# Performance work log

Measured on AMD Instinct MI355X. Metric: run time of the kernel, lower is better.

Reference implementation:

```python
import jax, jax.numpy as jnp
import numpy as np

B, C, H, W = 2, 256, 56, 56
NH = 8
HD = C // NH
SCALE = HD ** -0.5
BN_EPS = 1e-5


def _linear(x, w, b=None):
    y = jnp.einsum('...i,oi->...o', x, w)
    return y + b if b is not None else y


def _dwconv3(v, w, b):
    # depthwise 3x3, stride 1, pad 1
    y = jax.lax.conv_general_dilated(v, w, (1, 1), 'SAME',
                                     dimension_numbers=('NCHW', 'OIHW', 'NCHW'),
                                     feature_group_count=C)
    return y + b[None, :, None, None]


def _spectral(x, context, qw, kvw, pw, pb, dww, dwb):
    # SpectralCrossAttention, sr_ratio=1 path
    xt = jnp.transpose(x, (0, 2, 3, 1))                    # B,H,W,C
    q = jnp.transpose(_linear(xt, qw), (0, 3, 1, 2))       # B,C,H,W
    ct = jnp.transpose(context, (0, 2, 3, 1))
    kv = _linear(ct, kvw)                                  # B,H,W,2C -> split [2,C]
    k = jnp.transpose(kv[..., :C], (0, 3, 1, 2))
    v = jnp.transpose(kv[..., C:], (0, 3, 1, 2))
    v_local = _dwconv3(v, dww, dwb)
    qf = jnp.fft.rfft2(q, s=(H, W), axes=(-2, -1), norm='ortho')
    kf = jnp.fft.rfft2(k, s=(H, W), axes=(-2, -1), norm='ortho')
    attn_map = jnp.fft.irfft2(qf * kf, s=(H, W), axes=(-2, -1), norm='ortho')
    out = attn_map * v + v_local
    out = _linear(jnp.transpose(out, (0, 2, 3, 1)), pw, pb)
    return jnp.transpose(out, (0, 3, 1, 2))


def _token(x, context, qw, kvw, pw, pb, cw):
    # TokenSpectralResidualCrossAttention, sr_ratio=1 path (de_conv = Identity)
    N = H * W
    xt = jnp.transpose(x.reshape(B, C, N), (0, 2, 1))       # B,N,C
    ct = jnp.transpose(context.reshape(B, C, N), (0, 2, 1))
    q = jnp.transpose(_linear(xt, qw).reshape(B, N, NH, HD), (0, 2, 1, 3))  # B,NH,N,HD
    kv = _linear(ct, kvw).reshape(B, N, 2, NH, HD)
    k = jnp.transpose(kv[:, :, 0], (0, 2, 1, 3))
    v = jnp.transpose(kv[:, :, 1], (0, 2, 1, 3))            # B,NH,N,HD
    attn = jax.nn.softmax(jnp.einsum('bhnd,bhmd->bhnm', q, k) * SCALE, axis=-1)
    x_attn = jnp.transpose(jnp.einsum('bhnm,bhmd->bhnd', attn, v), (0, 2, 1, 3)).reshape(B, N, C)
    v_img = jnp.transpose(v, (0, 1, 3, 2)).reshape(B, C, H, W)
    vf = jnp.fft.rfft2(v_img, s=(H, W), axes=(-2, -1), norm='ortho')
    weight = cw[..., 0] + 1j * cw[..., 1]                   # C,H,W//2+1 complex
    v_res = jnp.fft.irfft2(vf * weight[None], s=(H, W), axes=(-2, -1), norm='ortho')
    v_res = jnp.transpose(v_res.reshape(B, C, N), (0, 2, 1))
    out = _linear(x_attn + v_res, pw, pb)
    return jnp.transpose(out, (0, 2, 1)).reshape(B, C, H, W)


def _fuse(os_, ot, g_w1, g_bn_g, g_bn_b, g_w2, g_b2):
    # spatial_gate: Conv1x1(2C->C, no bias) -> BN(eval: mean0/var1) -> ReLU -> Conv1x1(C->1) -> Sigmoid
    g_in = jnp.concatenate([os_, ot], axis=1)               # B,2C,H,W
    h = jnp.einsum('oc,bchw->bohw', g_w1, g_in)
    h = h / jnp.sqrt(1.0 + BN_EPS) * g_bn_g[None, :, None, None] + g_bn_b[None, :, None, None]
    h = jax.nn.relu(h)
    gate = jax.nn.sigmoid(jnp.einsum('oc,bchw->bohw', g_w2, h) + g_b2[None, :, None, None])
    return gate * os_ + (1.0 - gate) * ot


def setup_inputs():
    key = jax.random.key(0)
    ks = jax.random.split(key, 14)
    p = lambda i, shape, s=0.02: jax.random.normal(ks[i], shape, jnp.float32) * s
    return {
        'x': jax.random.normal(ks[0], (B, C, H, W), jnp.float32),
        'context': jax.random.normal(ks[1], (B, C, H, W), jnp.float32),
        's_q_w': p(2, (C, C)),
        's_kv_w': p(3, (2 * C, C)),
        's_proj_w': p(4, (C, C)),
        's_proj_b': jnp.zeros((C,), jnp.float32),
        's_dw_w': p(5, (C, 1, 3, 3), float(np.sqrt(2.0 / 9.0))),
        's_dw_b': jnp.zeros((C,), jnp.float32),
        't_q_w': p(6, (C, C)),
        't_kv_w': p(7, (2 * C, C)),
        't_proj_w': p(8, (C, C)),
        't_proj_b': jnp.zeros((C,), jnp.float32),
        't_cw': p(9, (C, H, W // 2 + 1, 2)),
        'g_w1': p(10, (C, 2 * C), float(np.sqrt(2.0 / C))),
        'g_bn_g': jnp.ones((C,), jnp.float32),
        'g_bn_b': jnp.zeros((C,), jnp.float32),
        'g_w2': p(11, (1, C), float(np.sqrt(2.0 / C))),
        'g_b2': jnp.zeros((1,), jnp.float32),
    }


def reference(x, context, s_q_w, s_kv_w, s_proj_w, s_proj_b, s_dw_w, s_dw_b,
              t_q_w, t_kv_w, t_proj_w, t_proj_b, t_cw,
              g_w1, g_bn_g, g_bn_b, g_w2, g_b2):
    os_ = _spectral(x, context, s_q_w, s_kv_w, s_proj_w, s_proj_b, s_dw_w, s_dw_b)
    ot = _token(x, context, t_q_w, t_kv_w, t_proj_w, t_proj_b, t_cw)
    return _fuse(os_, ot, g_w1, g_bn_g, g_bn_b, g_w2, g_b2)
```

## Files before the change

### kernel.cpp

```cpp
#include <hip/hip_runtime.h>

namespace {
constexpr int kB = 2;
constexpr int kC = 256;
constexpr int kH = 56;
constexpr int kW = 56;
constexpr int kN = kH * kW;
constexpr int kNH = 8;
constexpr int kHD = 32;
constexpr int kNF = kW / 2 + 1;
constexpr int kSpec = kH * kNF;
constexpr long kCN = (long)kC * kN;
constexpr float kAttScale = 0.17677669529663687f;
constexpr float kLog2e = 1.4426950408889634f;
constexpr float kAng = 6.283185307179586f / 56.0f;
constexpr int TW1F = 0;
constexpr int TW2F = 8192;
constexpr int TW1I = 12288;
constexpr int TW2I = 20480;
constexpr int TWTOT = 24576;
}

typedef __attribute__((ext_vector_type(8))) short short8;
typedef __attribute__((ext_vector_type(4))) float float4v;

union Frag {
    short8 s;
    unsigned short u[8];
    uint2 u2[2];
    uint4 u4;
};

__device__ __forceinline__ unsigned short f2b(float f) {
    unsigned u = __float_as_uint(f);
    return (unsigned short)((u + 0x7FFFu + ((u >> 16) & 1u)) >> 16);
}
__device__ __forceinline__ float b2f(unsigned short u) {
    return __uint_as_float((unsigned)u << 16);
}
__device__ __forceinline__ unsigned f2b_pk(float a, float b) {
    unsigned ua = __float_as_uint(a); ua = (ua + 0x7FFFu + ((ua >> 16) & 1u)) >> 16;
    unsigned ub = __float_as_uint(b); ub = (ub + 0x7FFFu + ((ub >> 16) & 1u)) >> 16;
    return ua | (ub << 16);
}
__device__ __forceinline__ unsigned pk_trunc(float a, float b) {
    return (__float_as_uint(a) >> 16) | (__float_as_uint(b) & 0xFFFF0000u);
}
__device__ __forceinline__ uint4 pk8(const float* v) {
    return make_uint4(f2b_pk(v[0], v[1]), f2b_pk(v[2], v[3]),
                      f2b_pk(v[4], v[5]), f2b_pk(v[6], v[7]));
}

__global__ __launch_bounds__(256)
void twiddle_init_kernel(unsigned short* __restrict__ tw)
{
    int idx = blockIdx.x * 256 + threadIdx.x;
    if (idx >= TWTOT) return;
    float val = 0.f;
    if (idx < TW2F) {
        int r = idx >> 6, c = idx & 63;
        if (c < 56) {
            if (r < 56)       val = cosf(kAng * (float)((r * c) % 56));
            else if (r < 112) val = sinf(kAng * (float)(((r - 56) * c) % 56));
        }
    } else if (idx < TW1I) {
        int t = idx - TW2F; int r = t >> 6, c = t & 63;
        if (c < 56) {
            if (r < 29)                  val = cosf(kAng * (float)((r * c) % 56));
            else if (r >= 32 && r < 61)  val = sinf(kAng * (float)(((r - 32) * c) % 56));
        }
    } else if (idx < TW2I) {
        int t = idx - TW1I; int r = t >> 6, c = t & 63;
        if (c < 56) {
            if (r < 56)                  val = cosf(kAng * (float)((r * c) % 56));
            else if (r >= 64 && r < 120) val = sinf(kAng * (float)(((r - 64) * c) % 56));
        }
    } else {
        int t = idx - TW2I; int x = t >> 6, c = t & 63;
        if (x < 56 && c < 58) {
            int v = c >> 1;
            float wv = ((v == 0) || (v == 28)) ? 1.f : 2.f;
            float a = kAng * (float)((v * x) % 56);
            val = (c & 1) ? (-wv * sinf(a)) : (wv * cosf(a));
        }
    }
    tw[idx] = f2b(val);
}

__device__ void dft_fwd_body(char* smem, int bx,
                             const float* __restrict__ s0, const float* __restrict__ s1,
                             const float* __restrict__ s2, float* __restrict__ d0,
                             float* __restrict__ d1, float* __restrict__ d2,
                             const unsigned short* __restrict__ tw)
{
    const int which = bx >> 9, ch = bx & 511;
    const int b = ch >> 8, c = ch & 255;
    const float* src; long stride; float* spec;
    if (which == 0)      { src = s0; stride = kCN;     spec = d0; }
    else if (which == 1) { src = s1; stride = 2 * kCN; spec = d1; }
    else                 { src = s2; stride = 2 * kCN; spec = d2; }
    const float* img = src + (long)b * stride + (long)c * kN;

    unsigned short (*Gb)[72]    = (unsigned short(*)[72])smem;
    unsigned short (*imgT)[72]  = (unsigned short(*)[72])(smem + 18432);
    unsigned short (*Yb)[116]   = (unsigned short(*)[116])(smem + 18432);

    const int tid = threadIdx.x;
    const int wave = tid >> 6, lane = tid & 63;
    const int ln = lane & 15, qd = lane >> 4;

    for (int i = tid; i < 64 * 72; i += 256) {
        int r = i / 72, cc = i - r * 72;
        if (r >= 56 || cc >= 56) imgT[r][cc] = 0;
    }
    for (int i = tid; i < kN; i += 256) {
        int y = i / 56, x = i - y * 56;
        imgT[x][y] = f2b(img[i]);
    }
    __syncthreads();

    float4v acc1[2][4];
#pragma unroll
    for (int m = 0; m < 2; ++m)
#pragma unroll
        for (int n = 0; n < 4; ++n) acc1[m][n] = (float4v){0.f, 0.f, 0.f, 0.f};
#pragma unroll
    for (int ks = 0; ks < 2; ++ks) {
        Frag a[2], bf[4];
#pragma unroll
        for (int m = 0; m < 2; ++m)
            a[m].u4 = *(const uint4*)(tw + TW1F + ((2 * wave + m) * 16 + ln) * 64 + ks * 32 + qd * 8);
#pragma unroll
        for (int n = 0; n < 4; ++n)
            bf[n].u4 = *(const uint4*)&imgT[n * 16 + ln][ks * 32 + qd * 8];
#pragma unroll
        for (int m = 0; m < 2; ++m)
#pragma unroll
            for (int n = 0; n < 4; ++n)
                acc1[m][n] = __builtin_amdgcn_mfma_f32_16x16x32_bf16(a[m].s, bf[n].s, acc1[m][n], 0, 0, 0);
    }
#pragma unroll
    for (int m = 0; m < 2; ++m)
#pragma unroll
        for (int n = 0; n < 4; ++n)
#pragma unroll
            for (int r = 0; r < 4; ++r)
                Gb[(2 * wave + m) * 16 + qd * 4 + r][n * 16 + ln] = f2b(acc1[m][n][r]);
    __syncthreads();

    float4v acc2[7];
#pragma unroll
    for (int n = 0; n < 7; ++n) acc2[n] = (float4v){0.f, 0.f, 0.f, 0.f};
#pragma unroll
    for (int ks = 0; ks < 2; ++ks) {
        Frag a;
        a.u4 = *(const uint4*)(tw + TW2F + (wave * 16 + ln) * 64 + ks * 32 + qd * 8);
#pragma unroll
        for (int n = 0; n < 7; ++n) {
            Frag bb;
            bb.u4 = *(const uint4*)&Gb[n * 16 + ln][ks * 32 + qd * 8];
            acc2[n] = __builtin_amdgcn_mfma_f32_16x16x32_bf16(a.s, bb.s, acc2[n], 0, 0, 0);
        }
    }
#pragma unroll
    for (int n = 0; n < 7; ++n)
#pragma unroll
        for (int r = 0; r < 4; ++r)
            Yb[wave * 16 + qd * 4 + r][n * 16 + ln] = f2b(acc2[n][r]);
    __syncthreads();

    float2* outp = (float2*)spec + (long)ch * kSpec;
    for (int i = tid; i < kSpec; i += 256) {
        int u = i / kNF, v = i - u * kNF;
        float Qr = b2f(Yb[v][u]) - b2f(Yb[32 + v][56 + u]);
        float Qi = -b2f(Yb[32 + v][u]) - b2f(Yb[v][56 + u]);
        outp[i] = make_float2(Qr, Qi);
    }
}

__device__ void prepack_body(char* smem, int blk, const float* __restrict__ tkv,
                             unsigned short* __restrict__ Kp,
                             unsigned short* __restrict__ Vp)
{
    const int i = blk % 49;
    const int h = (blk / 49) & 7;
    const int b = blk / (49 * 8);
    const float* kb = tkv + (long)b * 2 * kCN + (long)h * kHD * kN;
    const float* vb = kb + kCN;
    const int tid = threadIdx.x;

    float (*Ks)[72] = (float(*)[72])smem;
#pragma unroll
    for (int j = 0; j < 8; ++j) {
        int e = tid + j * 256;
        int d = e >> 6, c = e & 63;
        Ks[d][c] = kb[(long)d * kN + i * 64 + c];
    }
    __syncthreads();
    {
        int tl = tid >> 6, lnn = (tid >> 2) & 15, qdd = tid & 3;
        float v[8];
#pragma unroll
        for (int j = 0; j < 8; ++j) v[j] = Ks[qdd * 8 + j][tl * 16 + lnn];
        unsigned short* dst = Kp + ((long)(b * 8 + h) * 196 + 4 * i + tl) * 512 + lnn * 32 + qdd * 8;
        *(uint4*)dst = pk8(v);
    }
    {
        int g = tid >> 7, dh = (tid >> 6) & 1, lnn = (tid >> 2) & 15, qdd = tid & 3;
        int d = dh * 16 + lnn;
        const float* src = vb + (long)d * kN + i * 64 + g * 32 + qdd * 8;
        float v[8];
        *(float4*)&v[0] = *(const float4*)src;
        *(float4*)&v[4] = *(const float4*)(src + 4);
        unsigned short* dst = Vp + ((long)(b * 8 + h) * 49 + i) * 2048 + ((g * 2 + dh) * 16 + lnn) * 32 + qdd * 8;
        *(uint4*)dst = pk8(v);
    }
}

__global__ __launch_bounds__(256)
void fwd3_prepack_kernel(const float* __restrict__ s0, const float* __restrict__ s1,
                         const float* __restrict__ s2, float* __restrict__ d0,
                         float* __restrict__ d1, float* __restrict__ d2,
                         const unsigned short* __restrict__ tw,
                         const float* __restrict__ tkv,
                         unsigned short* __restrict__ Kp, unsigned short* __restrict__ Vp)
{
    __shared__ __align__(16) char smem[33280];
    if (blockIdx.x < 1536)
        dft_fwd_body(smem, blockIdx.x, s0, s1, s2, d0, d1, d2, tw);
    else
        prepack_body(smem, blockIdx.x - 1536, tkv, Kp, Vp);
}

__global__ __launch_bounds__(256)
void dft_inv_mfma2(const float* __restrict__ fQ, const float* __restrict__ fK,
                   const float* __restrict__ fV, const float* __restrict__ cw,
                   float* __restrict__ dst1, float* __restrict__ dst2,
                   const float* __restrict__ skvp, const float* __restrict__ dww,
                   const float* __restrict__ dwb, const unsigned short* __restrict__ tw)
{
    const int unit = blockIdx.x >> 9;
    const int ch = blockIdx.x & 511;
    const int b = ch >> 8, c = ch & 255;
    __shared__ __align__(16) char smem[27648];
    unsigned short (*Pb)[72]  = (unsigned short(*)[72])smem;
    unsigned short (*Yb)[72]  = (unsigned short(*)[72])(smem + 9216);
    unsigned short (*T2)[72]  = (unsigned short(*)[72])smem;
    float (*svs)[65]          = (float(*)[65])(smem + 9216);

    const int tid = threadIdx.x;
    const int wave = tid >> 6, lane = tid & 63;
    const int ln = lane & 15, qd = lane >> 4;

    const float2* Pin; const float2* Min; float scale; float* dst;
    if (unit == 0) {
        Pin = (const float2*)fQ + (long)ch * kSpec;
        Min = (const float2*)fK + (long)ch * kSpec;
        scale = 1.0f / 175616.0f; dst = dst1;
    } else {
        Pin = (const float2*)fV + (long)ch * kSpec;
        Min = (const float2*)cw + (long)c * kSpec;
        scale = 1.0f / 3136.0f; dst = dst2;
    }

    for (int i = tid; i < 64 * 72; i += 256) {
        int r = i / 72, cc = i - r * 72;
        if (r >= 58 || cc >= 56) Pb[r][cc] = 0;
    }
    for (int i = tid; i < kSpec; i += 256) {
        int u = i / kNF, v = i - u * kNF;
        float2 p = Pin[i];
        float2 m = Min[i];
        float pr = (p.x * m.x - p.y * m.y) * scale;
        float pi = (p.x * m.y + p.y * m.x) * scale;
        Pb[2 * v][u]     = f2b(pr);
        Pb[2 * v + 1][u] = f2b(pi);
    }
    __syncthreads();

    float4v acc1[2][4];
#pragma unroll
    for (int m = 0; m < 2; ++m)
#pragma unroll
        for (int n = 0; n < 4; ++n) acc1[m][n] = (float4v){0.f, 0.f, 0.f, 0.f};
#pragma unroll
    for (int ks = 0; ks < 2; ++ks) {
        Frag a[2], bf[4];
#pragma unroll
        for (int m = 0; m < 2; ++m)
            a[m].u4 = *(const uint4*)(tw + TW1I + ((2 * wave + m) * 16 + ln) * 64 + ks * 32 + qd * 8);
#pragma unroll
        for (int n = 0; n < 4; ++n)
            bf[n].u4 = *(const uint4*)&Pb[n * 16 + ln][ks * 32 + qd * 8];
#pragma unroll
        for (int m = 0; m < 2; ++m)
#pragma unroll
            for (int n = 0; n < 4; ++n)
                acc1[m][n] = __builtin_amdgcn_mfma_f32_16x16x32_bf16(a[m].s, bf[n].s, acc1[m][n], 0, 0, 0);
    }
#pragma unroll
    for (int m = 0; m < 2; ++m)
#pragma unroll
        for (int n = 0; n < 4; ++n)
#pragma unroll
            for (int r = 0; r < 4; ++r)
                Yb[(2 * wave + m) * 16 + qd * 4 + r][n * 16 + ln] = f2b(acc1[m][n][r]);
    __syncthreads();

    for (int i = tid; i < 64 * 72; i += 256) {
        int r = i / 72, cc = i - r * 72;
        if (r >= 56 || cc >= 58) T2[r][cc] = 0;
    }
    __syncthreads();
    for (int i = tid; i < 56 * kNF; i += 256) {
        int y = i / kNF, v = i - y * kNF;
        float Tr = b2f(Yb[y][2 * v])     - b2f(Yb[64 + y][2 * v + 1]);
        float Ti = b2f(Yb[y][2 * v + 1]) + b2f(Yb[64 + y][2 * v]);
        T2[y][2 * v]     = f2b(Tr);
        T2[y][2 * v + 1] = f2b(Ti);
    }
    __syncthreads();

    float wreg[9]; float bias = 0.f;
    if (unit == 0) {
        const float* svp = skvp + (long)b * 2 * kCN + kCN + (long)c * kN;
        for (int i = tid; i < 58 * 65; i += 256) {
            int y = i / 65, x = i - y * 65;
            if (y == 0 || y == 57 || x == 0 || x >= 57) ((float*)svs)[i] = 0.f;
        }
        for (int i = tid; i < kN; i += 256) {
            int y = i / 56, x = i - y * 56;
            svs[y + 1][x + 1] = svp[i];
        }
#pragma unroll
        for (int j = 0; j < 9; ++j) wreg[j] = dww[c * 9 + j];
        bias = dwb[c];
    }

    float4v acc2[4];
#pragma unroll
    for (int n = 0; n < 4; ++n) acc2[n] = (float4v){0.f, 0.f, 0.f, 0.f};
#pragma unroll
    for (int ks = 0; ks < 2; ++ks) {
        Frag a;
        a.u4 = *(const uint4*)(tw + TW2I + (wave * 16 + ln) * 64 + ks * 32 + qd * 8);
#pragma unroll
        for (int n = 0; n < 4; ++n) {
            Frag bb;
            bb.u4 = *(const uint4*)&T2[n * 16 + ln][ks * 32 + qd * 8];
            acc2[n] = __builtin_amdgcn_mfma_f32_16x16x32_bf16(a.s, bb.s, acc2[n], 0, 0, 0);
        }
    }
    __syncthreads();

    float* outd = dst + (long)ch * kN;
#pragma unroll
    for (int n = 0; n < 4; ++n) {
        int y = n * 16 + ln;
        if (y < 56) {
#pragma unroll
            for (int r = 0; r < 4; ++r) {
                int x = wave * 16 + qd * 4 + r;
                if (x < 56) {
                    int e = y * 56 + x;
                    if (unit == 0) {
                        float s = bias;
                        s = fmaf(wreg[0], svs[y][x],     s);
                        s = fmaf(wreg[1], svs[y][x + 1], s);
                        s = fmaf(wreg[2], svs[y][x + 2], s);
                        s = fmaf(wreg[3], svs[y + 1][x],     s);
                        s = fmaf(wreg[4], svs[y + 1][x + 1], s);
                        s = fmaf(wreg[5], svs[y + 1][x + 2], s);
                        s = fmaf(wreg[6], svs[y + 2][x],     s);
                        s = fmaf(wreg[7], svs[y + 2][x + 1], s);
                        s = fmaf(wreg[8], svs[y + 2][x + 2], s);
                        outd[e] = fmaf(acc2[n][r], svs[y + 1][x + 1], s);
                    } else {
                        outd[e] = acc2[n][r];
                    }
                }
            }
        }
    }
}

__global__ __launch_bounds__(256)
void gemm_fused(const float* __restrict__ W0, const float* __restrict__ W1,
                const float* __restrict__ X0, const float* __restrict__ X1,
                const float* __restrict__ b0, const float* __restrict__ b1,
                float* __restrict__ Y0, float* __restrict__ Y1,
                int oHalf, int CI, long xbs, long ybs, int oOffset)
{
    const int b  = blockIdx.z;
    const int sel = blockIdx.y >= oHalf;
    const int o0 = (sel ? blockIdx.y - oHalf : blockIdx.y) * 64;
    const int oY = o0 + (sel ? oOffset : 0);
    const int n0 = blockIdx.x * 128;
    const float* Wm = sel ? W1 : W0;
    const float* bias = sel ? b1 : b0;
    const float* Xb = (sel ? X1 : X0) + (long)b * xbs;
    float* Yb = (sel ? Y1 : Y0) + (long)b * ybs;

    __shared__ __align__(16) unsigned short Wt[64][40];
    __shared__ __align__(16) unsigned short Xt[128][40];

    const int tid = threadIdx.x;
    const int wave = tid >> 6, lane = tid & 63;
    const int ln = lane & 15, qd = lane >> 4;
    const int wy = wave >> 1, wx = wave & 1;

    const int ow = tid >> 2, kcw = tid & 3;
    const int nx = tid & 127, kcx = tid >> 7;
    const bool xvalid = (n0 + nx) < kN;

    float4v acc[2][4];
#pragma unroll
    for (int i = 0; i < 2; ++i)
#pragma unroll
        for (int j = 0; j < 4; ++j) acc[i][j] = (float4v){0.f, 0.f, 0.f, 0.f};

    float wpre[8], xpre[16];
    {
        const float* ws = Wm + (long)(o0 + ow) * CI + kcw * 8;
        *(float4*)&wpre[0] = *(const float4*)ws;
        *(float4*)&wpre[4] = *(const float4*)(ws + 4);
#pragma unroll
        for (int j = 0; j < 16; ++j)
            xpre[j] = xvalid ? Xb[(long)(kcx * 16 + j) * kN + n0 + nx] : 0.f;
    }

    for (int k0 = 0; k0 < CI; k0 += 32) {
        *(uint4*)&Wt[ow][kcw * 8]      = pk8(wpre);
        *(uint4*)&Xt[nx][kcx * 16]     = pk8(xpre);
        *(uint4*)&Xt[nx][kcx * 16 + 8] = pk8(xpre + 8);
        __syncthreads();

        if (k0 + 32 < CI) {
            const float* ws = Wm + (long)(o0 + ow) * CI + k0 + 32 + kcw * 8;
            *(float4*)&wpre[0] = *(const float4*)ws;
            *(float4*)&wpre[4] = *(const float4*)(ws + 4);
#pragma unroll
            for (int j = 0; j < 16; ++j)
                xpre[j] = xvalid ? Xb[(long)(k0 + 32 + kcx * 16 + j) * kN + n0 + nx] : 0.f;
        }

        Frag af[2], bf4[4];
#pragma unroll
        for (int mt = 0; mt < 2; ++mt)
            af[mt].u4 = *(const uint4*)&Wt[wy * 32 + mt * 16 + ln][qd * 8];
#pragma unroll
        for (int nt = 0; nt < 4; ++nt)
            bf4[nt].u4 = *(const uint4*)&Xt[wx * 64 + nt * 16 + ln][qd * 8];
#pragma unroll
        for (int mt = 0; mt < 2; ++mt)
#pragma unroll
            for (int nt = 0; nt < 4; ++nt)
                acc[mt][nt] = __builtin_amdgcn_mfma_f32_16x16x32_bf16(
                    af[mt].s, bf4[nt].s, acc[mt][nt], 0, 0, 0);
        __syncthreads();
    }

#pragma unroll
    for (int mt = 0; mt < 2; ++mt) {
        const int obL = o0 + wy * 32 + mt * 16 + qd * 4;
        const int obY = oY + wy * 32 + mt * 16 + qd * 4;
#pragma unroll
        for (int nt = 0; nt < 4; ++nt) {
            const int n = n0 + wx * 64 + nt * 16 + ln;
            if (n < kN) {
#pragma unroll
                for (int r = 0; r < 4; ++r) {
                    float v = acc[mt][nt][r];
                    if (bias) v += bias[obL + r];
                    Yb[(long)(obY + r) * kN + n] = v;
                }
            }
        }
    }
}

__global__ __launch_bounds__(256)
void gemm_bn_kernel(const float* __restrict__ Wm, const float* __restrict__ X,
                    const float* __restrict__ gamma, const float* __restrict__ beta,
                    float* __restrict__ Y, int CI, long xbs, long ybs)
{
    const int b  = blockIdx.z;
    const int o0 = blockIdx.y * 64;
    const int n0 = blockIdx.x * 128;
    const float* Xb = X + (long)b * xbs;
    float* Yb = Y + (long)b * ybs;

    __shared__ __align__(16) unsigned short Wt[64][40];
    __shared__ __align__(16) unsigned short Xt[128][40];

    const int tid = threadIdx.x;
    const int wave = tid >> 6, lane = tid & 63;
    const int ln = lane & 15, qd = lane >> 4;
    const int wy = wave >> 1, wx = wave & 1;

    const int ow = tid >> 2, kcw = tid & 3;
    const int nx = tid & 127, kcx = tid >> 7;
    const bool xvalid = (n0 + nx) < kN;

    float4v acc[2][4];
#pragma unroll
    for (int i = 0; i < 2; ++i)
#pragma unroll
        for (int j = 0; j < 4; ++j) acc[i][j] = (float4v){0.f, 0.f, 0.f, 0.f};

    float wpre[8], xpre[16];
    {
        const float* ws = Wm + (long)(o0 + ow) * CI + kcw * 8;
        *(float4*)&wpre[0] = *(const float4*)ws;
        *(float4*)&wpre[4] = *(const float4*)(ws + 4);
#pragma unroll
        for (int j = 0; j < 16; ++j)
            xpre[j] = xvalid ? Xb[(long)(kcx * 16 + j) * kN + n0 + nx] : 0.f;
    }

    for (int k0 = 0; k0 < CI; k0 += 32) {
        *(uint4*)&Wt[ow][kcw * 8]      = pk8(wpre);
        *(uint4*)&Xt[nx][kcx * 16]     = pk8(xpre);
        *(uint4*)&Xt[nx][kcx * 16 + 8] = pk8(xpre + 8);
        __syncthreads();

        if (k0 + 32 < CI) {
            const float* ws = Wm + (long)(o0 + ow) * CI + k0 + 32 + kcw * 8;
            *(float4*)&wpre[0] = *(const float4*)ws;
            *(float4*)&wpre[4] = *(const float4*)(ws + 4);
#pragma unroll
            for (int j = 0; j < 16; ++j)
                xpre[j] = xvalid ? Xb[(long)(k0 + 32 + kcx * 16 + j) * kN + n0 + nx] : 0.f;
        }

        Frag af[2], bf4[4];
#pragma unroll
        for (int mt = 0; mt < 2; ++mt)
            af[mt].u4 = *(const uint4*)&Wt[wy * 32 + mt * 16 + ln][qd * 8];
#pragma unroll
        for (int nt = 0; nt < 4; ++nt)
            bf4[nt].u4 = *(const uint4*)&Xt[wx * 64 + nt * 16 + ln][qd * 8];
#pragma unroll
        for (int mt = 0; mt < 2; ++mt)
#pragma unroll
            for (int nt = 0; nt < 4; ++nt)
                acc[mt][nt] = __builtin_amdgcn_mfma_f32_16x16x32_bf16(
                    af[mt].s, bf4[nt].s, acc[mt][nt], 0, 0, 0);
        __syncthreads();
    }

    const float rs = rsqrtf(1.0f + 1e-5f);
#pragma unroll
    for (int mt = 0; mt < 2; ++mt) {
        const int ob = o0 + wy * 32 + mt * 16 + qd * 4;
#pragma unroll
        for (int nt = 0; nt < 4; ++nt) {
            const int n = n0 + wx * 64 + nt * 16 + ln;
            if (n < kN) {
#pragma unroll
                for (int r = 0; r < 4; ++r) {
                    const int o = ob + r;
                    float v = fmaxf(fmaf(acc[mt][nt][r], gamma[o] * rs, beta[o]), 0.f);
                    Yb[(long)o * kN + n] = v;
                }
            }
        }
    }
}

__global__ __launch_bounds__(256, 4)
void attn_mfma_kernel(const float* __restrict__ tq,
                      const unsigned short* __restrict__ Kp,
                      const unsigned short* __restrict__ Vp,
                      float* __restrict__ Op, float* __restrict__ lp)
{
    const int bi = blockIdx.x;
    const int xcd = bi & 7;
    const int t = bi >> 3;
    const int gsel = (t >= 100) ? 1 : 0;
    const int r0 = t - gsel * 100;
    const int grpId = (gsel << 3) | xcd;
    const int b = grpId >> 3, h = grpId & 7;
    const int sp = r0 / 25;
    const int q0 = (r0 % 25) * 128;
    const int tid = threadIdx.x;
    const int wave = tid >> 6, lane = tid & 63;
    const int qd = lane >> 4, ln = lane & 15;
    const int i0 = (sp == 0) ? 0 : (12 * sp + 1);
    const int i1 = 12 * sp + 13;

    const float* qb = tq + (long)b * kCN + (long)h * kHD * kN;
    const unsigned short* KpB = Kp + (long)(b * 8 + h) * 196 * 512 + ln * 32 + qd * 8;
    const unsigned short* VpB = Vp + (long)(b * 8 + h) * 49 * 2048 + ln * 32 + qd * 8;

    __shared__ __align__(16) unsigned short Ps[4][32 * 40];
    unsigned short* PsW = Ps[wave];

    const float qscale = kAttScale * kLog2e;
    Frag qf[2];
#pragma unroll
    for (int qt = 0; qt < 2; ++qt) {
        int qg = q0 + wave * 32 + qt * 16 + ln;
        bool qv = qg < kN;
#pragma unroll
        for (int j = 0; j < 8; ++j) {
            int d = qd * 8 + j;
            float v = qv ? qb[(long)d * kN + qg] * qscale : 0.f;
            qf[qt].u[j] = f2b(v);
        }
    }

    float4v o[2][2];
#pragma unroll
    for (int qt = 0; qt < 2; ++qt)
#pragma unroll
        for (int dh = 0; dh < 2; ++dh) o[qt][dh] = (float4v){0.f, 0.f, 0.f, 0.f};
    float lsum[2] = {0.f, 0.f};

    unsigned W[4][2][2];
    Frag ka[4];
#pragma unroll
    for (int m = 0; m < 4; ++m)
        ka[m].u4 = *(const uint4*)(KpB + (long)(4 * i0 + m) * 512);

    auto computeW = [&]() {
#pragma unroll
        for (int m = 0; m < 4; ++m) {
            float4v s0 = __builtin_amdgcn_mfma_f32_16x16x32_bf16(
                ka[m].s, qf[0].s, (float4v){0.f, 0.f, 0.f, 0.f}, 0, 0, 0);
            float4v s1 = __builtin_amdgcn_mfma_f32_16x16x32_bf16(
                ka[m].s, qf[1].s, (float4v){0.f, 0.f, 0.f, 0.f}, 0, 0, 0);
            float a0 = __builtin_amdgcn_exp2f(s0[0]);
            float a1 = __builtin_amdgcn_exp2f(s0[1]);
            float a2 = __builtin_amdgcn_exp2f(s0[2]);
            float a3 = __builtin_amdgcn_exp2f(s0[3]);
            lsum[0] += (a0 + a1) + (a2 + a3);
            W[m][0][0] = pk_trunc(a0, a1);
            W[m][0][1] = pk_trunc(a2, a3);
            float b0 = __builtin_amdgcn_exp2f(s1[0]);
            float b1 = __builtin_amdgcn_exp2f(s1[1]);
            float b2 = __builtin_amdgcn_exp2f(s1[2]);
            float b3 = __builtin_amdgcn_exp2f(s1[3]);
            lsum[1] += (b0 + b1) + (b2 + b3);
            W[m][1][0] = pk_trunc(b0, b1);
            W[m][1][1] = pk_trunc(b2, b3);
        }
    };

    computeW();
    if (i0 + 1 < i1) {
#pragma unroll
        for (int m = 0; m < 4; ++m)
            ka[m].u4 = *(const uint4*)(KpB + (long)(4 * (i0 + 1) + m) * 512);
    }

    for (int i = i0; i < i1; ++i) {
        Frag va[2][2];
#pragma unroll
        for (int g = 0; g < 2; ++g)
#pragma unroll
            for (int dh = 0; dh < 2; ++dh)
                va[g][dh].u4 = *(const uint4*)(VpB + (long)i * 2048 + (g * 2 + dh) * 512);

#pragma unroll
        for (int m = 0; m < 4; ++m)
#pragma unroll
            for (int qt = 0; qt < 2; ++qt)
                *(uint2*)&PsW[(qt * 16 + ln) * 40 + m * 16 + qd * 4] =
                    make_uint2(W[m][qt][0], W[m][qt][1]);

        if (i + 1 < i1) {
            computeW();
            if (i + 2 < i1) {
#pragma unroll
                for (int m = 0; m < 4; ++m)
                    ka[m].u4 = *(const uint4*)(KpB + (long)(4 * (i + 2) + m) * 512);
            }
        }

#pragma unroll
        for (int g = 0; g < 2; ++g) {
            Frag pa[2];
#pragma unroll
            for (int qt = 0; qt < 2; ++qt)
                pa[qt].u4 = *(const uint4*)&PsW[(qt * 16 + ln) * 40 + g * 32 + qd * 8];
#pragma unroll
            for (int qt = 0; qt < 2; ++qt)
#pragma unroll
                for (int dh = 0; dh < 2; ++dh)
                    o[qt][dh] = __builtin_amdgcn_mfma_f32_16x16x32_bf16(
                        pa[qt].s, va[g][dh].s, o[qt][dh], 0, 0, 0);
        }
    }

    const long grp = (long)(sp * 16 + b * 8 + h);
#pragma unroll
    for (int qt = 0; qt < 2; ++qt) {
        lsum[qt] += __shfl_xor(lsum[qt], 16, 64);
        lsum[qt] += __shfl_xor(lsum[qt], 32, 64);
        if (qd == 0)
            lp[grp * 3200 + q0 + wave * 32 + qt * 16 + ln] = lsum[qt];
#pragma unroll
        for (int dh = 0; dh < 2; ++dh)
#pragma unroll
            for (int r = 0; r < 4; ++r) {
                int q = q0 + wave * 32 + qt * 16 + qd * 4 + r;
                Op[(grp * 3200 + q) * 32 + dh * 16 + ln] = o[qt][dh][r];
            }
    }
}

__global__ __launch_bounds__(256)
void attn_combine_kernel(const float* __restrict__ Op, const float* __restrict__ lp,
                         float* __restrict__ xo)
{
    const int qc = blockIdx.x, bh = blockIdx.y;
    const int b = bh >> 3, h = bh & 7;
    const int q0 = qc * 64;
    __shared__ float T[32][65];
    const int tid = threadIdx.x;

    for (int i = tid; i < 64 * 32; i += 256) {
        int ql = i >> 5, d = i & 31;
        float ov = 0.f, l = 0.f;
#pragma unroll
        for (int s = 0; s < 4; ++s) {
            long g = (long)(s * 16 + bh);
            ov += Op[(g * 3200 + q0 + ql) * 32 + d];
            l  += lp[g * 3200 + q0 + ql];
        }
        T[d][ql] = ov / l;
    }
    __syncthreads();
    for (int i = tid; i < 32 * 64; i += 256) {
        int d = i >> 6, ql = i & 63;
        xo[(long)b * kCN + (long)(h * kHD + d) * kN + q0 + ql] += T[d][ql];
    }
}

__global__ __launch_bounds__(256)
void gateblend_kernel(const float* __restrict__ hbuf, const float* __restrict__ w2,
                      const float* __restrict__ b2, const float* __restrict__ gcat,
                      float* __restrict__ out)
{
    const int n0 = blockIdx.x * 64;
    const int b = blockIdx.y;
    const int lane = threadIdx.x & 63;
    const int g = threadIdx.x >> 6;
    const float* hb = hbuf + (long)b * kCN + n0 + lane;
    float s = 0.f;
#pragma unroll 8
    for (int c = g * 64; c < g * 64 + 64; ++c)
        s = fmaf(w2[c], hb[(long)c * kN], s);
    __shared__ float red[4][64];
    __shared__ float sgate[64];
    red[g][lane] = s;
    __syncthreads();
    if (g == 0) {
        float t = red[0][lane] + red[1][lane] + red[2][lane] + red[3][lane];
        sgate[lane] = 1.f / (1.f + __expf(-(t + b2[0])));
    }
    __syncthreads();
    const float gt = sgate[lane];
    const float* osp = gcat + (long)b * 2 * kCN + n0 + lane;
    const float* otp = osp + kCN;
    float* op = out + (long)b * kCN + n0 + lane;
    for (int c = g; c < kC; c += 4) {
        float os = osp[(long)c * kN];
        float ot = otp[(long)c * kN];
        op[(long)c * kN] = gt * os + (1.f - gt) * ot;
    }
}

extern "C" void kernel_launch(void* const* d_in, const int* in_sizes, int n_in,
                              void* d_out, int out_size, void* d_ws, size_t ws_size,
                              hipStream_t stream)
{
    const float* x      = (const float*)d_in[0];
    const float* ctx    = (const float*)d_in[1];
    const float* s_q_w  = (const float*)d_in[2];
    const float* s_kv_w = (const float*)d_in[3];
    const float* s_p_w  = (const float*)d_in[4];
    const float* s_p_b  = (const float*)d_in[5];
    const float* s_dw_w = (const float*)d_in[6];
    const float* s_dw_b = (const float*)d_in[7];
    const float* t_q_w  = (const float*)d_in[8];
    const float* t_kv_w = (const float*)d_in[9];
    const float* t_p_w  = (const float*)d_in[10];
    const float* t_p_b  = (const float*)d_in[11];
    const float* t_cw   = (const float*)d_in[12];
    const float* g_w1   = (const float*)d_in[13];
    const float* g_bn_g = (const float*)d_in[14];
    const float* g_bn_b = (const float*)d_in[15];
    const float* g_w2   = (const float*)d_in[16];
    const float* g_b2   = (const float*)d_in[17];
    float* out = (float*)d_out;

    float* ws = (float*)d_ws;
    const long SPEC2 = (long)kB * kC * kSpec * 2;
    float* sq   = ws;
    float* skv  = sq   + kB * kCN;
    float* tq   = skv  + kB * 2 * kCN;
    float* tkv  = tq   + kB * kCN;
    float* vloc = tkv  + kB * 2 * kCN;
    float* fQ   = vloc + kB * kCN;
    float* fK   = fQ   + SPEC2;
    float* fV   = fK   + SPEC2;
    float* gcat = fV   + SPEC2;
    float* gate = gcat + kB * 2 * kCN;
    unsigned short* tw = (unsigned short*)(gate + kB * kN);
    unsigned short* Kp = tw + TWTOT;
    unsigned short* Vp = Kp + (long)16 * 196 * 512;
    float* Opart = (float*)(Vp + (long)16 * 49 * 2048);
    float* lpart = Opart + (long)64 * 3200 * 32;

    dim3 blk(256, 1, 1);

    twiddle_init_kernel<<<dim3(TWTOT / 256), blk, 0, stream>>>(tw);

    gemm_fused<<<dim3(25, 8, kB), blk, 0, stream>>>(
        s_q_w, t_q_w, x, x, nullptr, nullptr, sq, tq, 4, kC, kCN, kCN, 0);
    gemm_fused<<<dim3(25, 16, kB), blk, 0, stream>>>(
        s_kv_w, t_kv_w, ctx, ctx, nullptr, nullptr, skv, tkv, 8, kC, kCN, 2 * kCN, 0);

    fwd3_prepack_kernel<<<dim3(3 * kB * kC + kB * kNH * 49), blk, 0, stream>>>(
        sq, skv, tkv + kCN, fQ, fK, fV, tw, tkv, Kp, Vp);

    dft_inv_mfma2<<<dim3(2 * kB * kC), blk, 0, stream>>>(
        fQ, fK, fV, t_cw, vloc, sq, skv, s_dw_w, s_dw_b, tw);

    attn_mfma_kernel<<<dim3(1600), blk, 0, stream>>>(tq, Kp, Vp, Opart, lpart);
    attn_combine_kernel<<<dim3(49, 16), blk, 0, stream>>>(Opart, lpart, sq);

    gemm_fused<<<dim3(25, 8, kB), blk, 0, stream>>>(
        s_p_w, t_p_w, vloc, sq, s_p_b, t_p_b, gcat, gcat, 4, kC, kCN, 2 * kCN, 256);

    gemm_bn_kernel<<<dim3(25, 4, kB), blk, 0, stream>>>(g_w1, gcat, g_bn_g, g_bn_b, tkv, 2 * kC, 2 * kCN, kCN);
    gateblend_kernel<<<dim3(49, kB), blk, 0, stream>>>(tkv, g_w2, g_b2, gcat, out);
}
```

Before: 280.4 us.

## Merge twiddle init with projections and inverse DFT with attention into combined launches

Twiddle-table generation and the q/kv projection GEMMs now run as block ranges of one launch, and the inverse-DFT blocks are interleaved with the attention blocks in a second combined launch. The aim is fewer kernel launches and letting independent work fill the GPU together, instead of leaving tail gaps between dependent launches. In exchange, the combined inverse-DFT/attention kernel carries the larger shared-memory footprint and launch_bounds(256,4) for both paths, which may limit occupancy or register allocation for the DFT part. The GEMM body was factored into a shared device function.

New measurement: 266.1 us, median of 2. 1.05x faster.

```diff
diff --git a/kernel.cpp b/kernel.cpp
--- a/kernel.cpp
+++ b/kernel.cpp
@@ -51,10 +51,9 @@
                       f2b_pk(v[4], v[5]), f2b_pk(v[6], v[7]));
 }
 
-__global__ __launch_bounds__(256)
-void twiddle_init_kernel(unsigned short* __restrict__ tw)
-{
-    int idx = blockIdx.x * 256 + threadIdx.x;
+__device__ void twiddle_body(int blk, unsigned short* __restrict__ tw)
+{
+    int idx = blk * 256 + threadIdx.x;
     if (idx >= TWTOT) return;
     float val = 0.f;
     if (idx < TW2F) {
@@ -85,6 +84,119 @@
         }
     }
     tw[idx] = f2b(val);
+}
+
+__device__ void gemm_bias_body(char* smem, const float* __restrict__ Wm,
+                               const float* __restrict__ Xb,
+                               const float* __restrict__ bias, float* __restrict__ Yb,
+                               int o0, int oY, int n0, int CI)
+{
+    unsigned short (*Wt)[40] = (unsigned short(*)[40])smem;
+    unsigned short (*Xt)[40] = (unsigned short(*)[40])(smem + 5120);
+
+    const int tid = threadIdx.x;
+    const int wave = tid >> 6, lane = tid & 63;
+    const int ln = lane & 15, qd = lane >> 4;
+    const int wy = wave >> 1, wx = wave & 1;
+
+    const int ow = tid >> 2, kcw = tid & 3;
+    const int nx = tid & 127, kcx = tid >> 7;
+    const bool xvalid = (n0 + nx) < kN;
+
+    float4v acc[2][4];
+#pragma unroll
+    for (int i = 0; i < 2; ++i)
+#pragma unroll
+        for (int j = 0; j < 4; ++j) acc[i][j] = (float4v){0.f, 0.f, 0.f, 0.f};
+
+    float wpre[8], xpre[16];
+    {
+        const float* ws = Wm + (long)(o0 + ow) * CI + kcw * 8;
+        *(float4*)&wpre[0] = *(const float4*)ws;
+        *(float4*)&wpre[4] = *(const float4*)(ws + 4);
+#pragma unroll
+        for (int j = 0; j < 16; ++j)
+            xpre[j] = xvalid ? Xb[(long)(kcx * 16 + j) * kN + n0 + nx] : 0.f;
+    }
+
+    for (int k0 = 0; k0 < CI; k0 += 32) {
+        *(uint4*)&Wt[ow][kcw * 8]      = pk8(wpre);
+        *(uint4*)&Xt[nx][kcx * 16]     = pk8(xpre);
+        *(uint4*)&Xt[nx][kcx * 16 + 8] = pk8(xpre + 8);
+        __syncthreads();
+
+        if (k0 + 32 < CI) {
+            const float* ws = Wm + (long)(o0 + ow) * CI + k0 + 32 + kcw * 8;
+            *(float4*)&wpre[0] = *(const float4*)ws;
+            *(float4*)&wpre[4] = *(const float4*)(ws + 4);
+#pragma unroll
+            for (int j = 0; j < 16; ++j)
+                xpre[j] = xvalid ? Xb[(long)(k0 + 32 + kcx * 16 + j) * kN + n0 + nx] : 0.f;
+        }
+
+        Frag af[2], bf4[4];
+#pragma unroll
+        for (int mt = 0; mt < 2; ++mt)
+            af[mt].u4 = *(const uint4*)&Wt[wy * 32 + mt * 16 + ln][qd * 8];
+#pragma unroll
+        for (int nt = 0; nt < 4; ++nt)
+            bf4[nt].u4 = *(const uint4*)&Xt[wx * 64 + nt * 16 + ln][qd * 8];
+#pragma unroll
+        for (int mt = 0; mt < 2; ++mt)
+#pragma unroll
+            for (int nt = 0; nt < 4; ++nt)
+                acc[mt][nt] = __builtin_amdgcn_mfma_f32_16x16x32_bf16(
+                    af[mt].s, bf4[nt].s, acc[mt][nt], 0, 0, 0);
+        __syncthreads();
+    }
+
+#pragma unroll
+    for (int mt = 0; mt < 2; ++mt) {
+        const int obL = o0 + wy * 32 + mt * 16 + qd * 4;
+        const int obY = oY + wy * 32 + mt * 16 + qd * 4;
+#pragma unroll
+        for (int nt = 0; nt < 4; ++nt) {
+            const int n = n0 + wx * 64 + nt * 16 + ln;
+            if (n < kN) {
+#pragma unroll
+                for (int r = 0; r < 4; ++r) {
+                    float v = acc[mt][nt][r];
+                    if (bias) v += bias[obL + r];
+                    Yb[(long)(obY + r) * kN + n] = v;
+                }
+            }
+        }
+    }
+}
+
+__global__ __launch_bounds__(256)
+void init_proj_kernel(unsigned short* __restrict__ tw,
+                      const float* __restrict__ x, const float* __restrict__ ctx,
+                      const float* __restrict__ s_q_w, const float* __restrict__ t_q_w,
+                      const float* __restrict__ s_kv_w, const float* __restrict__ t_kv_w,
+                      float* __restrict__ sq, float* __restrict__ tq,
+                      float* __restrict__ skv, float* __restrict__ tkv)
+{
+    __shared__ __align__(16) char smem[15360];
+    int bi = blockIdx.x;
+    if (bi < 96) { twiddle_body(bi, tw); return; }
+    bi -= 96;
+    if (bi < 400) {
+        int b = bi / 200, rem = bi % 200;
+        int y = rem / 25, xb = rem % 25;
+        int sel = y >= 4;
+        int o0 = (sel ? y - 4 : y) * 64;
+        gemm_bias_body(smem, sel ? t_q_w : s_q_w, (x + (long)b * kCN), nullptr,
+                       (sel ? tq : sq) + (long)b * kCN, o0, o0, xb * 128, kC);
+    } else {
+        bi -= 400;
+        int b = bi / 400, rem = bi % 400;
+        int y = rem / 25, xb = rem % 25;
+        int sel = y >= 8;
+        int o0 = (sel ? y - 8 : y) * 64;
+        gemm_bias_body(smem, sel ? t_kv_w : s_kv_w, (ctx + (long)b * kCN), nullptr,
+                       (sel ? tkv : skv) + (long)b * 2 * kCN, o0, o0, xb * 128, kC);
+    }
 }
 
 __device__ void dft_fwd_body(char* smem, int bx,
@@ -232,17 +344,16 @@
         prepack_body(smem, blockIdx.x - 1536, tkv, Kp, Vp);
 }
 
-__global__ __launch_bounds__(256)
-void dft_inv_mfma2(const float* __restrict__ fQ, const float* __restrict__ fK,
-                   const float* __restrict__ fV, const float* __restrict__ cw,
-                   float* __restrict__ dst1, float* __restrict__ dst2,
-                   const float* __restrict__ skvp, const float* __restrict__ dww,
-                   const float* __restrict__ dwb, const unsigned short* __restrict__ tw)
-{
-    const int unit = blockIdx.x >> 9;
-    const int ch = blockIdx.x & 511;
+__device__ void dft_inv_body(char* smem, int bx,
+                             const float* __restrict__ fQ, const float* __restrict__ fK,
+                             const float* __restrict__ fV, const float* __restrict__ cw,
+                             float* __restrict__ dst1, float* __restrict__ dst2,
+                             const float* __restrict__ skvp, const float* __restrict__ dww,
+                             const float* __restrict__ dwb, const unsigned short* __restrict__ tw)
+{
+    const int unit = bx >> 9;
+    const int ch = bx & 511;
     const int b = ch >> 8, c = ch & 255;
-    __shared__ __align__(16) char smem[27648];
     unsigned short (*Pb)[72]  = (unsigned short(*)[72])smem;
     unsigned short (*Yb)[72]  = (unsigned short(*)[72])(smem + 9216);
     unsigned short (*T2)[72]  = (unsigned short(*)[72])smem;
@@ -384,199 +495,14 @@
     }
 }
 
-__global__ __launch_bounds__(256)
-void gemm_fused(const float* __restrict__ W0, const float* __restrict__ W1,
-                const float* __restrict__ X0, const float* __restrict__ X1,
-                const float* __restrict__ b0, const float* __restrict__ b1,
-                float* __restrict__ Y0, float* __restrict__ Y1,
-                int oHalf, int CI, long xbs, long ybs, int oOffset)
-{
-    const int b  = blockIdx.z;
-    const int sel = blockIdx.y >= oHalf;
-    const int o0 = (sel ? blockIdx.y - oHalf : blockIdx.y) * 64;
-    const int oY = o0 + (sel ? oOffset : 0);
-    const int n0 = blockIdx.x * 128;
-    const float* Wm = sel ? W1 : W0;
-    const float* bias = sel ? b1 : b0;
-    const float* Xb = (sel ? X1 : X0) + (long)b * xbs;
-    float* Yb = (sel ? Y1 : Y0) + (long)b * ybs;
-
-    __shared__ __align__(16) unsigned short Wt[64][40];
-    __shared__ __align__(16) unsigned short Xt[128][40];
-
-    const int tid = threadIdx.x;
-    const int wave = tid >> 6, lane = tid & 63;
-    const int ln = lane & 15, qd = lane >> 4;
-    const int wy = wave >> 1, wx = wave & 1;
-
-    const int ow = tid >> 2, kcw = tid & 3;
-    const int nx = tid & 127, kcx = tid >> 7;
-    const bool xvalid = (n0 + nx) < kN;
-
-    float4v acc[2][4];
-#pragma unroll
-    for (int i = 0; i < 2; ++i)
-#pragma unroll
-        for (int j = 0; j < 4; ++j) acc[i][j] = (float4v){0.f, 0.f, 0.f, 0.f};
-
-    float wpre[8], xpre[16];
-    {
-        const float* ws = Wm + (long)(o0 + ow) * CI + kcw * 8;
-        *(float4*)&wpre[0] = *(const float4*)ws;
-        *(float4*)&wpre[4] = *(const float4*)(ws + 4);
-#pragma unroll
-        for (int j = 0; j < 16; ++j)
-            xpre[j] = xvalid ? Xb[(long)(kcx * 16 + j) * kN + n0 + nx] : 0.f;
-    }
-
-    for (int k0 = 0; k0 < CI; k0 += 32) {
-        *(uint4*)&Wt[ow][kcw * 8]      = pk8(wpre);
-        *(uint4*)&Xt[nx][kcx * 16]     = pk8(xpre);
-        *(uint4*)&Xt[nx][kcx * 16 + 8] = pk8(xpre + 8);
-        __syncthreads();
-
-        if (k0 + 32 < CI) {
-            const float* ws = Wm + (long)(o0 + ow) * CI + k0 + 32 + kcw * 8;
-            *(float4*)&wpre[0] = *(const float4*)ws;
-            *(float4*)&wpre[4] = *(const float4*)(ws + 4);
-#pragma unroll
-            for (int j = 0; j < 16; ++j)
-                xpre[j] = xvalid ? Xb[(long)(k0 + 32 + kcx * 16 + j) * kN + n0 + nx] : 0.f;
-        }
-
-        Frag af[2], bf4[4];
-#pragma unroll
-        for (int mt = 0; mt < 2; ++mt)
-            af[mt].u4 = *(const uint4*)&Wt[wy * 32 + mt * 16 + ln][qd * 8];
-#pragma unroll
-        for (int nt = 0; nt < 4; ++nt)
-            bf4[nt].u4 = *(const uint4*)&Xt[wx * 64 + nt * 16 + ln][qd * 8];
-#pragma unroll
-        for (int mt = 0; mt < 2; ++mt)
-#pragma unroll
-            for (int nt = 0; nt < 4; ++nt)
-                acc[mt][nt] = __builtin_amdgcn_mfma_f32_16x16x32_bf16(
-                    af[mt].s, bf4[nt].s, acc[mt][nt], 0, 0, 0);
-        __syncthreads();
-    }
-
-#pragma unroll
-    for (int mt = 0; mt < 2; ++mt) {
-        const int obL = o0 + wy * 32 + mt * 16 + qd * 4;
-        const int obY = oY + wy * 32 + mt * 16 + qd * 4;
-#pragma unroll
-        for (int nt = 0; nt < 4; ++nt) {
-            const int n = n0 + wx * 64 + nt * 16 + ln;
-            if (n < kN) {
-#pragma unroll
-                for (int r = 0; r < 4; ++r) {
-                    float v = acc[mt][nt][r];
-                    if (bias) v += bias[obL + r];
-                    Yb[(long)(obY + r) * kN + n] = v;
-                }
-            }
-        }
-    }
-}
-
-__global__ __launch_bounds__(256)
-void gemm_bn_kernel(const float* __restrict__ Wm, const float* __restrict__ X,
-                    const float* __restrict__ gamma, const float* __restrict__ beta,
-                    float* __restrict__ Y, int CI, long xbs, long ybs)
-{
-    const int b  = blockIdx.z;
-    const int o0 = blockIdx.y * 64;
-    const int n0 = blockIdx.x * 128;
-    const float* Xb = X + (long)b * xbs;
-    float* Yb = Y + (long)b * ybs;
-
-    __shared__ __align__(16) unsigned short Wt[64][40];
-    __shared__ __align__(16) unsigned short Xt[128][40];
-
-    const int tid = threadIdx.x;
-    const int wave = tid >> 6, lane = tid & 63;
-    const int ln = lane & 15, qd = lane >> 4;
-    const int wy = wave >> 1, wx = wave & 1;
-
-    const int ow = tid >> 2, kcw = tid & 3;
-    const int nx = tid & 127, kcx = tid >> 7;
-    const bool xvalid = (n0 + nx) < kN;
-
-    float4v acc[2][4];
-#pragma unroll
-    for (int i = 0; i < 2; ++i)
-#pragma unroll
-        for (int j = 0; j < 4; ++j) acc[i][j] = (float4v){0.f, 0.f, 0.f, 0.f};
-
-    float wpre[8], xpre[16];
-    {
-        const float* ws = Wm + (long)(o0 + ow) * CI + kcw * 8;
-        *(float4*)&wpre[0] = *(const float4*)ws;
-        *(float4*)&wpre[4] = *(const float4*)(ws + 4);
-#pragma unroll
-        for (int j = 0; j < 16; ++j)
-            xpre[j] = xvalid ? Xb[(long)(kcx * 16 + j) * kN + n0 + nx] : 0.f;
-    }
-
-    for (int k0 = 0; k0 < CI; k0 += 32) {
-        *(uint4*)&Wt[ow][kcw * 8]      = pk8(wpre);
-        *(uint4*)&Xt[nx][kcx * 16]     = pk8(xpre);
-        *(uint4*)&Xt[nx][kcx * 16 + 8] = pk8(xpre + 8);
-        __syncthreads();
-
-        if (k0 + 32 < CI) {
-            const float* ws = Wm + (long)(o0 + ow) * CI + k0 + 32 + kcw * 8;
-            *(float4*)&wpre[0] = *(const float4*)ws;
-            *(float4*)&wpre[4] = *(const float4*)(ws + 4);
-#pragma unroll
-            for (int j = 0; j < 16; ++j)
-                xpre[j] = xvalid ? Xb[(long)(k0 + 32 + kcx * 16 + j) * kN + n0 + nx] : 0.f;
-        }
-
-        Frag af[2], bf4[4];
-#pragma unroll
-        for (int mt = 0; mt < 2; ++mt)
-            af[mt].u4 = *(const uint4*)&Wt[wy * 32 + mt * 16 + ln][qd * 8];
-#pragma unroll
-        for (int nt = 0; nt < 4; ++nt)
-            bf4[nt].u4 = *(const uint4*)&Xt[wx * 64 + nt * 16 + ln][qd * 8];
-#pragma unroll
-        for (int mt = 0; mt < 2; ++mt)
-#pragma unroll
-            for (int nt = 0; nt < 4; ++nt)
-                acc[mt][nt] = __builtin_amdgcn_mfma_f32_16x16x32_bf16(
-                    af[mt].s, bf4[nt].s, acc[mt][nt], 0, 0, 0);
-        __syncthreads();
-    }
-
-    const float rs = rsqrtf(1.0f + 1e-5f);
-#pragma unroll
-    for (int mt = 0; mt < 2; ++mt) {
-        const int ob = o0 + wy * 32 + mt * 16 + qd * 4;
-#pragma unroll
-        for (int nt = 0; nt < 4; ++nt) {
-            const int n = n0 + wx * 64 + nt * 16 + ln;
-            if (n < kN) {
-#pragma unroll
-                for (int r = 0; r < 4; ++r) {
-                    const int o = ob + r;
-                    float v = fmaxf(fmaf(acc[mt][nt][r], gamma[o] * rs, beta[o]), 0.f);
-                    Yb[(long)o * kN + n] = v;
-                }
-            }
-        }
-    }
-}
-
-__global__ __launch_bounds__(256, 4)
-void attn_mfma_kernel(const float* __restrict__ tq,
-                      const unsigned short* __restrict__ Kp,
-                      const unsigned short* __restrict__ Vp,
-                      float* __restrict__ Op, float* __restrict__ lp)
-{
-    const int bi = blockIdx.x;
-    const int xcd = bi & 7;
-    const int t = bi >> 3;
+__device__ void attn_body(char* smem, int abi,
+                          const float* __restrict__ tq,
+                          const unsigned short* __restrict__ Kp,
+                          const unsigned short* __restrict__ Vp,
+                          float* __restrict__ Op, float* __restrict__ lp)
+{
+    const int xcd = abi & 7;
+    const int t = abi >> 3;
     const int gsel = (t >= 100) ? 1 : 0;
     const int r0 = t - gsel * 100;
     const int grpId = (gsel << 3) | xcd;
@@ -593,8 +519,7 @@
     const unsigned short* KpB = Kp + (long)(b * 8 + h) * 196 * 512 + ln * 32 + qd * 8;
     const unsigned short* VpB = Vp + (long)(b * 8 + h) * 49 * 2048 + ln * 32 + qd * 8;
 
-    __shared__ __align__(16) unsigned short Ps[4][32 * 40];
-    unsigned short* PsW = Ps[wave];
+    unsigned short* PsW = (unsigned short*)smem + wave * (32 * 40);
 
     const float qscale = kAttScale * kLog2e;
     Frag qf[2];
@@ -710,6 +635,26 @@
     }
 }
 
+__global__ __launch_bounds__(256, 4)
+void inv_attn_kernel(const float* __restrict__ fQ, const float* __restrict__ fK,
+                     const float* __restrict__ fV, const float* __restrict__ cw,
+                     float* __restrict__ dst1, float* __restrict__ dst2,
+                     const float* __restrict__ skvp, const float* __restrict__ dww,
+                     const float* __restrict__ dwb, const unsigned short* __restrict__ tw,
+                     const float* __restrict__ tq,
+                     const unsigned short* __restrict__ Kp,
+                     const unsigned short* __restrict__ Vp,
+                     float* __restrict__ Op, float* __restrict__ lp)
+{
+    __shared__ __align__(16) char smem[27648];
+    const int per = blockIdx.x / 328;
+    const int off = blockIdx.x % 328;
+    if (off < 128)
+        dft_inv_body(smem, per * 128 + off, fQ, fK, fV, cw, dst1, dst2, skvp, dww, dwb, tw);
+    else
+        attn_body(smem, per * 200 + (off - 128), tq, Kp, Vp, Op, lp);
+}
+
 __global__ __launch_bounds__(256)
 void attn_combine_kernel(const float* __restrict__ Op, const float* __restrict__ lp,
                          float* __restrict__ xo)
@@ -735,6 +680,112 @@
     for (int i = tid; i < 32 * 64; i += 256) {
         int d = i >> 6, ql = i & 63;
         xo[(long)b * kCN + (long)(h * kHD + d) * kN + q0 + ql] += T[d][ql];
+    }
+}
+
+__global__ __launch_bounds__(256)
+void gemm_fused(const float* __restrict__ W0, const float* __restrict__ W1,
+                const float* __restrict__ X0, const float* __restrict__ X1,
+                const float* __restrict__ b0, const float* __restrict__ b1,
+                float* __restrict__ Y0, float* __restrict__ Y1,
+                int oHalf, int CI, long xbs, long ybs, int oOffset)
+{
+    __shared__ __align__(16) char smem[15360];
+    const int b  = blockIdx.z;
+    const int sel = blockIdx.y >= oHalf;
+    const int o0 = (sel ? blockIdx.y - oHalf : blockIdx.y) * 64;
+    const int oY = o0 + (sel ? oOffset : 0);
+    gemm_bias_body(smem, sel ? W1 : W0, (sel ? X1 : X0) + (long)b * xbs,
+                   sel ? b1 : b0, (sel ? Y1 : Y0) + (long)b * ybs,
+                   o0, oY, blockIdx.x * 128, CI);
+}
+
+__global__ __launch_bounds__(256)
+void gemm_bn_kernel(const float* __restrict__ Wm, const float* __restrict__ X,
+                    const float* __restrict__ gamma, const float* __restrict__ beta,
+                    float* __restrict__ Y, int CI, long xbs, long ybs)
+{
+    const int b  = blockIdx.z;
+    const int o0 = blockIdx.y * 64;
+    const int n0 = blockIdx.x * 128;
+    const float* Xb = X + (long)b * xbs;
+    float* Yb = Y + (long)b * ybs;
+
+    __shared__ __align__(16) unsigned short Wt[64][40];
+    __shared__ __align__(16) unsigned short Xt[128][40];
+
+    const int tid = threadIdx.x;
+    const int wave = tid >> 6, lane = tid & 63;
+    const int ln = lane & 15, qd = lane >> 4;
+    const int wy = wave >> 1, wx = wave & 1;
+
+    const int ow = tid >> 2, kcw = tid & 3;
+    const int nx = tid & 127, kcx = tid >> 7;
+    const bool xvalid = (n0 + nx) < kN;
+
+    float4v acc[2][4];
+#pragma unroll
+    for (int i = 0; i < 2; ++i)
+#pragma unroll
+        for (int j = 0; j < 4; ++j) acc[i][j] = (float4v){0.f, 0.f, 0.f, 0.f};
+
+    float wpre[8], xpre[16];
+    {
+        const float* ws = Wm + (long)(o0 + ow) * CI + kcw * 8;
+        *(float4*)&wpre[0] = *(const float4*)ws;
+        *(float4*)&wpre[4] = *(const float4*)(ws + 4);
+#pragma unroll
+        for (int j = 0; j < 16; ++j)
+            xpre[j] = xvalid ? Xb[(long)(kcx * 16 + j) * kN + n0 + nx] : 0.f;
+    }
+
+    for (int k0 = 0; k0 < CI; k0 += 32) {
+        *(uint4*)&Wt[ow][kcw * 8]      = pk8(wpre);
+        *(uint4*)&Xt[nx][kcx * 16]     = pk8(xpre);
+        *(uint4*)&Xt[nx][kcx * 16 + 8] = pk8(xpre + 8);
+        __syncthreads();
+
+        if (k0 + 32 < CI) {
+            const float* ws = Wm + (long)(o0 + ow) * CI + k0 + 32 + kcw * 8;
+            *(float4*)&wpre[0] = *(const float4*)ws;
+            *(float4*)&wpre[4] = *(const float4*)(ws + 4);
+#pragma unroll
+            for (int j = 0; j < 16; ++j)
+                xpre[j] = xvalid ? Xb[(long)(k0 + 32 + kcx * 16 + j) * kN + n0 + nx] : 0.f;
+        }
+
+        Frag af[2], bf4[4];
+#pragma unroll
+        for (int mt = 0; mt < 2; ++mt)
+            af[mt].u4 = *(const uint4*)&Wt[wy * 32 + mt * 16 + ln][qd * 8];
+#pragma unroll
+        for (int nt = 0; nt < 4; ++nt)
+            bf4[nt].u4 = *(const uint4*)&Xt[wx * 64 + nt * 16 + ln][qd * 8];
+#pragma unroll
+        for (int mt = 0; mt < 2; ++mt)
+#pragma unroll
+            for (int nt = 0; nt < 4; ++nt)
+                acc[mt][nt] = __builtin_amdgcn_mfma_f32_16x16x32_bf16(
+                    af[mt].s, bf4[nt].s, acc[mt][nt], 0, 0, 0);
+        __syncthreads();
+    }
+
+    const float rs = rsqrtf(1.0f + 1e-5f);
+#pragma unroll
+    for (int mt = 0; mt < 2; ++mt) {
+        const int ob = o0 + wy * 32 + mt * 16 + qd * 4;
+#pragma unroll
+        for (int nt = 0; nt < 4; ++nt) {
+            const int n = n0 + wx * 64 + nt * 16 + ln;
+            if (n < kN) {
+#pragma unroll
+                for (int r = 0; r < 4; ++r) {
+                    const int o = ob + r;
+                    float v = fmaxf(fmaf(acc[mt][nt][r], gamma[o] * rs, beta[o]), 0.f);
+                    Yb[(long)o * kN + n] = v;
+                }
+            }
+        }
     }
 }
 
@@ -816,25 +867,22 @@
 
     dim3 blk(256, 1, 1);
 
-    twiddle_init_kernel<<<dim3(TWTOT / 256), blk, 0, stream>>>(tw);
-
-    gemm_fused<<<dim3(25, 8, kB), blk, 0, stream>>>(
-        s_q_w, t_q_w, x, x, nullptr, nullptr, sq, tq, 4, kC, kCN, kCN, 0);
-    gemm_fused<<<dim3(25, 16, kB), blk, 0, stream>>>(
-        s_kv_w, t_kv_w, ctx, ctx, nullptr, nullptr, skv, tkv, 8, kC, kCN, 2 * kCN, 0);
+    init_proj_kernel<<<dim3(1296), blk, 0, stream>>>(
+        tw, x, ctx, s_q_w, t_q_w, s_kv_w, t_kv_w, sq, tq, skv, tkv);
 
     fwd3_prepack_kernel<<<dim3(3 * kB * kC + kB * kNH * 49), blk, 0, stream>>>(
         sq, skv, tkv + kCN, fQ, fK, fV, tw, tkv, Kp, Vp);
 
-    dft_inv_mfma2<<<dim3(2 * kB * kC), blk, 0, stream>>>(
-        fQ, fK, fV, t_cw, vloc, sq, skv, s_dw_w, s_dw_b, tw);
-
-    attn_mfma_kernel<<<dim3(1600), blk, 0, stream>>>(tq, Kp, Vp, Opart, lpart);
+    inv_attn_kernel<<<dim3(2624), blk, 0, stream>>>(
+        fQ, fK, fV, t_cw, vloc, sq, skv, s_dw_w, s_dw_b, tw,
+        tq, Kp, Vp, Opart, lpart);
+
     attn_combine_kernel<<<dim3(49, 16), blk, 0, stream>>>(Opart, lpart, sq);
 
     gemm_fused<<<dim3(25, 8, kB), blk, 0, stream>>>(
         s_p_w, t_p_w, vloc, sq, s_p_b, t_p_b, gcat, gcat, 4, kC, kCN, 2 * kCN, 256);
 
     gemm_bn_kernel<<<dim3(25, 4, kB), blk, 0, stream>>>(g_w1, gcat, g_bn_g, g_bn_b, tkv, 2 * kC, 2 * kCN, kCN);
+
     gateblend_kernel<<<dim3(49, kB), blk, 0, stream>>>(tkv, g_w2, g_b2, gcat, out);
 }
```
